# Kernel optimization log

Measured on AMD Instinct MI355X. Metric: run time of the kernel, lower is better.

## Reference

```python
import jax, jax.numpy as jnp
import numpy as np

DIM = 1024
LN_EPS = 1e-5


def setup_inputs() -> dict:
    key = jax.random.key(0)
    ks = jax.random.split(key, 6)
    B, S, D = 8, 2048, DIM
    x = jax.random.normal(ks[0], (B, S, D), dtype=jnp.float32)
    mask = jnp.ones((B, S, 1), dtype=jnp.float32)
    # LayerNorm params
    ln_g = jnp.ones((D,), dtype=jnp.float32)
    ln_b = jnp.zeros((D,), dtype=jnp.float32)
    # FeedForward: Linear(D, D) -> GELU -> Linear(D, D); hidden_dim == dim per source
    lim = 1.0 / np.sqrt(D)
    w1 = jax.random.uniform(ks[1], (D, D), jnp.float32, -lim, lim)
    b1 = jax.random.uniform(ks[2], (D,), jnp.float32, -lim, lim)
    w2 = jax.random.uniform(ks[3], (D, D), jnp.float32, -lim, lim)
    b2 = jax.random.uniform(ks[4], (D,), jnp.float32, -lim, lim)
    return {"x": x, "mask": mask, "ln_g": ln_g, "ln_b": ln_b,
            "w1": w1, "b1": b1, "w2": w2, "b2": b2}


def _layernorm(t, g, b):
    mu = jnp.mean(t, axis=-1, keepdims=True)
    var = jnp.mean(jnp.square(t - mu), axis=-1, keepdims=True)
    return (t - mu) * jax.lax.rsqrt(var + LN_EPS) * g + b


def reference(x, mask, ln_g, ln_b, w1, b1, w2, b2):
    # torch.fft(t, signal_ndim=1): FFT over hidden axis (complex input, imag=0)
    ft = jnp.fft.fft(x.astype(jnp.float32), axis=-1)
    # torch.fft(., signal_ndim=2): 2D FFT over (seq, hidden)
    ft = jnp.fft.fft2(ft, axes=(-2, -1))
    ft = ft.real  # [..., 0] slice of the fake-complex tensor
    t = _layernorm(x + ft, ln_g, ln_b)
    # FeedForward: Linear -> GELU(exact) -> Linear (dropout is identity at eval)
    h = jax.nn.gelu(t @ w1 + b1, approximate=False)
    out = h @ w2 + b2
    return out * mask
```

## Files before the change

kernel.cpp:

```cpp
#include <hip/hip_runtime.h>
#include <math.h>

#define DIMD 1024
#define SEQ  2048
#define BATCH 8
#define ROWS (BATCH * SEQ)

#define MF 1152
#define KF 1088

typedef __attribute__((ext_vector_type(8))) short bf16x8;
typedef __attribute__((ext_vector_type(4))) float f32x4;
typedef __attribute__((ext_vector_type(8))) unsigned short ushort8;

__device__ __forceinline__ unsigned short f2bf(float f) {
    unsigned u = __float_as_uint(f);
    unsigned r = (u + 0x7FFFu + ((u >> 16) & 1u)) >> 16;
    return (unsigned short)r;
}
__device__ __forceinline__ void gl_lds16(const void* g, void* l) {
    __builtin_amdgcn_global_load_lds(
        (const __attribute__((address_space(1))) unsigned int*)g,
        (__attribute__((address_space(3))) unsigned int*)l, 16, 0, 0);
}


__global__ __launch_bounds__(256) void build_acos(unsigned short* __restrict__ Acos) {
    int s = blockIdx.x;
    for (int t = threadIdx.x; t < KF; t += 256) {
        float c = 0.0f;
        if (t <= 1024) {
            int prod = (s * t) & (SEQ - 1);
            c = cospif((float)prod * (1.0f / 1024.0f));
        }
        Acos[(size_t)s * KF + t] = f2bf(c);
    }
}

__global__ __launch_bounds__(256) void build_xe(const float* __restrict__ x,
                                                unsigned short* __restrict__ Xe) {
    int lane = threadIdx.x & 63;
    int oct  = threadIdx.x >> 6;
    int n = blockIdx.x * 64 + lane;
    int b = n >> 10, d = n & 1023;
    int rd = (DIMD - d) & (DIMD - 1);
    int t0 = blockIdx.y * 32 + oct * 8;
    const float* xb = x + (size_t)b * SEQ * DIMD + rd;
    ushort8 tmp;
    #pragma unroll
    for (int j = 0; j < 8; ++j) {
        int t = t0 + j;
        float v;
        if (t == 0)          v = xb[0];
        else if (t < 1024)   v = xb[(size_t)t * DIMD] + xb[(size_t)(2048 - t) * DIMD];
        else if (t == 1024)  v = xb[(size_t)1024 * DIMD];
        else                 v = 0.0f;
        tmp[j] = f2bf(v);
    }
    *(ushort8*)&Xe[(size_t)n * KF + t0] = tmp;
}

__global__ __launch_bounds__(256) void pack_wt(const float* __restrict__ W,
                                               unsigned short* __restrict__ Wt) {
    int lane = threadIdx.x & 63;
    int oct = threadIdx.x >> 6;
    int n = blockIdx.x * 64 + lane;
    int k0 = blockIdx.y * 32 + oct * 8;
    ushort8 tmp;
    #pragma unroll
    for (int j = 0; j < 8; ++j) tmp[j] = f2bf(W[(size_t)(k0 + j) * DIMD + n]);
    *(ushort8*)&Wt[(size_t)n * DIMD + k0] = tmp;
}

template <int MODE>
__global__ __launch_bounds__(256) void gemm_bt(const unsigned short* __restrict__ A,
                                               const unsigned short* __restrict__ B,
                                               int K, int lda, int ldb, int ldc,
                                               const float* __restrict__ bias,
                                               const float* __restrict__ mask,
                                               void* __restrict__ outp) {
    __shared__ unsigned short As[128 * 64];
    __shared__ unsigned short Bs[128 * 64];

    const int tid = threadIdx.x;
    const int lane = tid & 63;
    const int wv = tid >> 6;
    const int wm = wv & 1;
    const int wn = wv >> 1;
    const int fr = lane & 15;
    const int quad = lane >> 4;

    const int m0 = blockIdx.y * 128;
    const int n0 = blockIdx.x * 128;

    const int st_row = (lane >> 3);
    const int st_col = (lane & 7) * 8;

    f32x4 acc[4][4] = {};

    for (int k0 = 0; k0 < K; k0 += 64) {
        __syncthreads();
        #pragma unroll
        for (int i = 0; i < 4; ++i) {
            int chunk = wv * 4 + i;
            int ar = m0 + chunk * 8 + st_row;
            int br = n0 + chunk * 8 + st_row;
            gl_lds16(&A[(size_t)ar * lda + k0 + st_col], &As[chunk * 512]);
            gl_lds16(&B[(size_t)br * ldb + k0 + st_col], &Bs[chunk * 512]);
        }
        __syncthreads();

        #pragma unroll
        for (int ks = 0; ks < 2; ++ks) {
            bf16x8 af[4], bfv[4];
            #pragma unroll
            for (int i = 0; i < 4; ++i)
                af[i] = *(const bf16x8*)&As[(wm * 64 + i * 16 + fr) * 64 + ks * 32 + quad * 8];
            #pragma unroll
            for (int j = 0; j < 4; ++j)
                bfv[j] = *(const bf16x8*)&Bs[(wn * 64 + j * 16 + fr) * 64 + ks * 32 + quad * 8];
            #pragma unroll
            for (int i = 0; i < 4; ++i)
                #pragma unroll
                for (int j = 0; j < 4; ++j)
                    acc[i][j] = __builtin_amdgcn_mfma_f32_16x16x32_bf16(af[i], bfv[j], acc[i][j], 0, 0, 0);
        }
    }

    #pragma unroll
    for (int i = 0; i < 4; ++i) {
        int rowb = m0 + wm * 64 + i * 16 + quad * 4;
        #pragma unroll
        for (int j = 0; j < 4; ++j) {
            int col = n0 + wn * 64 + j * 16 + fr;
            #pragma unroll
            for (int r = 0; r < 4; ++r) {
                float v = acc[i][j][r];
                int row = rowb + r;
                if (MODE == 0) {
                    ((float*)outp)[(size_t)row * ldc + col] = v;
                } else if (MODE == 1) {
                    v += bias[col];
                    v = 0.5f * v * (1.0f + erff(v * 0.70710678118654752f));
                    ((unsigned short*)outp)[(size_t)row * ldc + col] = f2bf(v);
                } else {
                    v += bias[col];
                    v *= mask[row];
                    ((float*)outp)[(size_t)row * ldc + col] = v;
                }
            }
        }
    }
}

__global__ __launch_bounds__(256) void ln_mirror(const float* __restrict__ x,
                                                 const float* __restrict__ F,
                                                 const float* __restrict__ g,
                                                 const float* __restrict__ beta,
                                                 unsigned short* __restrict__ t) {
    const int row = blockIdx.x;
    const int b = row >> 11, s = row & 2047;
    const int sp = (s <= 1024) ? s : (2048 - s);

    float4 xv = ((const float4*)(x + (size_t)row * DIMD))[threadIdx.x];
    float4 fv = ((const float4*)(F + (size_t)sp * 8192 + (size_t)b * 1024))[threadIdx.x];
    float4 v;
    v.x = xv.x + 1024.0f * fv.x;
    v.y = xv.y + 1024.0f * fv.y;
    v.z = xv.z + 1024.0f * fv.z;
    v.w = xv.w + 1024.0f * fv.w;

    __shared__ float red[4];
    const int wave = threadIdx.x >> 6;
    const int lane = threadIdx.x & 63;

    float sm = v.x + v.y + v.z + v.w;
    #pragma unroll
    for (int off = 32; off > 0; off >>= 1) sm += __shfl_down(sm, off, 64);
    if (lane == 0) red[wave] = sm;
    __syncthreads();
    const float mean = (red[0] + red[1] + red[2] + red[3]) * (1.0f / DIMD);

    float dx0 = v.x - mean, dx1 = v.y - mean, dx2 = v.z - mean, dx3 = v.w - mean;
    float q = dx0 * dx0 + dx1 * dx1 + dx2 * dx2 + dx3 * dx3;
    __syncthreads();
    #pragma unroll
    for (int off = 32; off > 0; off >>= 1) q += __shfl_down(q, off, 64);
    if (lane == 0) red[wave] = q;
    __syncthreads();
    const float var = (red[0] + red[1] + red[2] + red[3]) * (1.0f / DIMD);
    const float rstd = rsqrtf(var + 1e-5f);

    float4 g4 = ((const float4*)g)[threadIdx.x];
    float4 b4 = ((const float4*)beta)[threadIdx.x];
    ushort4 o;
    o.x = f2bf(dx0 * rstd * g4.x + b4.x);
    o.y = f2bf(dx1 * rstd * g4.y + b4.y);
    o.z = f2bf(dx2 * rstd * g4.z + b4.z);
    o.w = f2bf(dx3 * rstd * g4.w + b4.w);
    ((ushort4*)(t + (size_t)row * DIMD))[threadIdx.x] = o;
}

#define BM 64
#define BN 64
#define BK 16

__global__ __launch_bounds__(256) void fft_cos_kernel(const float* __restrict__ x,
                                                      float* __restrict__ y) {
    __shared__ float tab[SEQ];
    __shared__ float As[BM][BK + 1];
    __shared__ float Bs[BK][BN + 1];
    const int tid = threadIdx.x;
    const int b = blockIdx.z;
    const int s0 = blockIdx.y * BM;
    const int n0 = blockIdx.x * BN;
    for (int i = tid; i < SEQ; i += 256) tab[i] = cospif((float)i * (1.0f / 1024.0f));
    const int tx = tid & 15;
    const int ty = tid >> 4;
    float acc[4][4] = {};
    const float* Xb = x + (size_t)b * SEQ * DIMD;
    for (int k0 = 0; k0 < SEQ; k0 += BK) {
        __syncthreads();
        for (int f = tid; f < BM * BK; f += 256) {
            int i = f / BK, k = f % BK;
            int prod = (s0 + i) * (k0 + k);
            As[i][k] = tab[prod & (SEQ - 1)];
        }
        for (int f = tid; f < BK * BN; f += 256) {
            int k = f / BN, j = f % BN;
            int d = n0 + j;
            int rd = (DIMD - d) & (DIMD - 1);
            Bs[k][j] = Xb[(size_t)(k0 + k) * DIMD + rd];
        }
        __syncthreads();
        #pragma unroll
        for (int k = 0; k < BK; ++k) {
            float a[4], bv[4];
            #pragma unroll
            for (int i = 0; i < 4; ++i) a[i] = As[ty * 4 + i][k];
            #pragma unroll
            for (int j = 0; j < 4; ++j) bv[j] = Bs[k][tx * 4 + j];
            #pragma unroll
            for (int i = 0; i < 4; ++i)
                #pragma unroll
                for (int j = 0; j < 4; ++j) acc[i][j] += a[i] * bv[j];
        }
    }
    #pragma unroll
    for (int i = 0; i < 4; ++i) {
        int s = s0 + ty * 4 + i;
        #pragma unroll
        for (int j = 0; j < 4; ++j) {
            int d = n0 + tx * 4 + j;
            y[((size_t)b * SEQ + s) * DIMD + d] = Xb[(size_t)s * DIMD + d] + 1024.0f * acc[i][j];
        }
    }
}

__global__ __launch_bounds__(256) void ln_kernel(float* __restrict__ y,
                                                 const float* __restrict__ g,
                                                 const float* __restrict__ beta) {
    const int row = blockIdx.x;
    float4* p = (float4*)(y + (size_t)row * DIMD);
    float4 v = p[threadIdx.x];
    __shared__ float red[4];
    const int wave = threadIdx.x >> 6;
    const int lane = threadIdx.x & 63;
    float s = v.x + v.y + v.z + v.w;
    #pragma unroll
    for (int off = 32; off > 0; off >>= 1) s += __shfl_down(s, off, 64);
    if (lane == 0) red[wave] = s;
    __syncthreads();
    const float mean = (red[0] + red[1] + red[2] + red[3]) * (1.0f / DIMD);
    float dx0 = v.x - mean, dx1 = v.y - mean, dx2 = v.z - mean, dx3 = v.w - mean;
    float q = dx0 * dx0 + dx1 * dx1 + dx2 * dx2 + dx3 * dx3;
    __syncthreads();
    #pragma unroll
    for (int off = 32; off > 0; off >>= 1) q += __shfl_down(q, off, 64);
    if (lane == 0) red[wave] = q;
    __syncthreads();
    const float var = (red[0] + red[1] + red[2] + red[3]) * (1.0f / DIMD);
    const float rstd = rsqrtf(var + 1e-5f);
    float4 g4 = ((const float4*)g)[threadIdx.x];
    float4 b4 = ((const float4*)beta)[threadIdx.x];
    float4 o;
    o.x = dx0 * rstd * g4.x + b4.x;
    o.y = dx1 * rstd * g4.y + b4.y;
    o.z = dx2 * rstd * g4.z + b4.z;
    o.w = dx3 * rstd * g4.w + b4.w;
    p[threadIdx.x] = o;
}

template <int MODE>
__global__ __launch_bounds__(256) void ff_gemm(const float* __restrict__ A,
                                               const float* __restrict__ W,
                                               const float* __restrict__ bias,
                                               const float* __restrict__ mask,
                                               float* __restrict__ out) {
    __shared__ float As[BM][BK + 1];
    __shared__ float Bs[BK][BN + 1];
    const int tid = threadIdx.x;
    const int tx = tid & 15;
    const int ty = tid >> 4;
    const int m0 = blockIdx.y * BM;
    const int n0 = blockIdx.x * BN;
    float acc[4][4] = {};
    for (int k0 = 0; k0 < DIMD; k0 += BK) {
        __syncthreads();
        for (int f = tid; f < BM * BK; f += 256) {
            int i = f / BK, k = f % BK;
            As[i][k] = A[(size_t)(m0 + i) * DIMD + k0 + k];
        }
        for (int f = tid; f < BK * BN; f += 256) {
            int k = f / BN, j = f % BN;
            Bs[k][j] = W[(size_t)(k0 + k) * DIMD + n0 + j];
        }
        __syncthreads();
        #pragma unroll
        for (int k = 0; k < BK; ++k) {
            float a[4], bv[4];
            #pragma unroll
            for (int i = 0; i < 4; ++i) a[i] = As[ty * 4 + i][k];
            #pragma unroll
            for (int j = 0; j < 4; ++j) bv[j] = Bs[k][tx * 4 + j];
            #pragma unroll
            for (int i = 0; i < 4; ++i)
                #pragma unroll
                for (int j = 0; j < 4; ++j) acc[i][j] += a[i] * bv[j];
        }
    }
    #pragma unroll
    for (int i = 0; i < 4; ++i) {
        int m = m0 + ty * 4 + i;
        float mk = (MODE == 1) ? mask[m] : 1.0f;
        #pragma unroll
        for (int j = 0; j < 4; ++j) {
            int n = n0 + tx * 4 + j;
            float v = acc[i][j] + bias[n];
            if (MODE == 0) v = 0.5f * v * (1.0f + erff(v * 0.70710678118654752f));
            else v *= mk;
            out[(size_t)m * DIMD + n] = v;
        }
    }
}

extern "C" void kernel_launch(void* const* d_in, const int* in_sizes, int n_in,
                              void* d_out, int out_size, void* d_ws, size_t ws_size,
                              hipStream_t stream) {
    const float* x    = (const float*)d_in[0];
    const float* mask = (const float*)d_in[1];
    const float* ln_g = (const float*)d_in[2];
    const float* ln_b = (const float*)d_in[3];
    const float* w1   = (const float*)d_in[4];
    const float* b1   = (const float*)d_in[5];
    const float* w2   = (const float*)d_in[6];
    const float* b2   = (const float*)d_in[7];
    float* out = (float*)d_out;

    const size_t MB = 1024 * 1024;
    dim3 blk(256);

    if (ws_size >= 70 * MB) {
        char* w = (char*)d_ws;
        unsigned short* Acos = (unsigned short*)w;
        unsigned short* Xe   = (unsigned short*)(w + 4 * MB);
        unsigned short* t    = (unsigned short*)(w + 32 * MB);
        unsigned short* W1t  = (unsigned short*)(w + 64 * MB);
        unsigned short* W2t  = (unsigned short*)(w + 66 * MB);
        unsigned short* h    = (unsigned short*)w;
        float* F = (float*)d_out;

        build_acos<<<dim3(MF), blk, 0, stream>>>(Acos);
        build_xe<<<dim3(8192 / 64, KF / 32), blk, 0, stream>>>(x, Xe);
        pack_wt<<<dim3(1024 / 64, 1024 / 32), blk, 0, stream>>>(w1, W1t);
        pack_wt<<<dim3(1024 / 64, 1024 / 32), blk, 0, stream>>>(w2, W2t);

        gemm_bt<0><<<dim3(8192 / 128, MF / 128), blk, 0, stream>>>(
            Acos, Xe, KF, KF, KF, 8192, nullptr, nullptr, F);
        ln_mirror<<<dim3(ROWS), blk, 0, stream>>>(x, F, ln_g, ln_b, t);
        gemm_bt<1><<<dim3(1024 / 128, ROWS / 128), blk, 0, stream>>>(
            t, W1t, 1024, 1024, 1024, 1024, b1, nullptr, h);
        gemm_bt<2><<<dim3(1024 / 128, ROWS / 128), blk, 0, stream>>>(
            h, W2t, 1024, 1024, 1024, 1024, b2, mask, out);
    } else {
        float* y = (float*)d_ws;
        const size_t bufBytes = (size_t)ROWS * DIMD * sizeof(float);
        fft_cos_kernel<<<dim3(DIMD / BN, SEQ / BM, BATCH), blk, 0, stream>>>(x, y);
        ln_kernel<<<dim3(ROWS), blk, 0, stream>>>(y, ln_g, ln_b);
        ff_gemm<0><<<dim3(DIMD / BN, ROWS / BM), blk, 0, stream>>>(y, w1, b1, nullptr, out);
        ff_gemm<1><<<dim3(DIMD / BN, ROWS / BM), blk, 0, stream>>>(out, w2, b2, mask, y);
        hipMemcpyAsync(d_out, y, bufBytes, hipMemcpyDeviceToDevice, stream);
    }
}
```

Measured before the change: 344.6 us.

## Fuse residual add and mirror expansion into DFT GEMM epilogue with bf16 output

The DFT GEMM epilogue now adds the input residual scaled spectrum directly and writes both the row and its mirrored row as bf16. This removes the fp32 intermediate F buffer and its re-read in LayerNorm, which now only reads a bf16 row. The FFN GEMMs also get a grouped block index remap to improve L2 reuse of A tiles. The trade-offs are that the pre-LN activations are rounded to bf16, and that the epilogue does scattered loads of x with narrow 16-bit stores.

Measured after the change: 380.4 us. 1.1x slower.

```diff
diff --git a/kernel.cpp b/kernel.cpp
--- a/kernel.cpp
+++ b/kernel.cpp
@@ -17,6 +17,9 @@
     unsigned u = __float_as_uint(f);
     unsigned r = (u + 0x7FFFu + ((u >> 16) & 1u)) >> 16;
     return (unsigned short)r;
+}
+__device__ __forceinline__ float bf2f(unsigned short h) {
+    return __uint_as_float(((unsigned)h) << 16);
 }
 __device__ __forceinline__ void gl_lds16(const void* g, void* l) {
     __builtin_amdgcn_global_load_lds(
@@ -76,6 +79,7 @@
 __global__ __launch_bounds__(256) void gemm_bt(const unsigned short* __restrict__ A,
                                                const unsigned short* __restrict__ B,
                                                int K, int lda, int ldb, int ldc,
+                                               const float* __restrict__ xres,
                                                const float* __restrict__ bias,
                                                const float* __restrict__ mask,
                                                void* __restrict__ outp) {
@@ -90,8 +94,16 @@
     const int fr = lane & 15;
     const int quad = lane >> 4;
 
-    const int m0 = blockIdx.y * 128;
-    const int n0 = blockIdx.x * 128;
+    int bx = blockIdx.x, by = blockIdx.y;
+    if (MODE != 0) {
+        int lin = bx + 8 * by;
+        int c = lin & 7;
+        int g = lin >> 3;
+        bx = g & 7;
+        by = (g >> 3) * 8 + c;
+    }
+    const int m0 = by * 128;
+    const int n0 = bx * 128;
 
     const int st_row = (lane >> 3);
     const int st_col = (lane & 7) * 8;
@@ -138,7 +150,17 @@
                 float v = acc[i][j][r];
                 int row = rowb + r;
                 if (MODE == 0) {
-                    ((float*)outp)[(size_t)row * ldc + col] = v;
+                    int s = row;
+                    if (s <= 1024) {
+                        int b = col >> 10, d = col & 1023;
+                        unsigned short* y = (unsigned short*)outp;
+                        size_t i1 = ((size_t)b * SEQ + s) * DIMD + d;
+                        y[i1] = f2bf(xres[i1] + 1024.0f * v);
+                        if (s >= 1 && s <= 1023) {
+                            size_t i2 = ((size_t)b * SEQ + (2048 - s)) * DIMD + d;
+                            y[i2] = f2bf(xres[i2] + 1024.0f * v);
+                        }
+                    }
                 } else if (MODE == 1) {
                     v += bias[col];
                     v = 0.5f * v * (1.0f + erff(v * 0.70710678118654752f));
@@ -153,35 +175,26 @@
     }
 }
 
-__global__ __launch_bounds__(256) void ln_mirror(const float* __restrict__ x,
-                                                 const float* __restrict__ F,
-                                                 const float* __restrict__ g,
-                                                 const float* __restrict__ beta,
-                                                 unsigned short* __restrict__ t) {
+__global__ __launch_bounds__(256) void ln_bf(const unsigned short* __restrict__ y,
+                                             const float* __restrict__ g,
+                                             const float* __restrict__ beta,
+                                             unsigned short* __restrict__ t) {
     const int row = blockIdx.x;
-    const int b = row >> 11, s = row & 2047;
-    const int sp = (s <= 1024) ? s : (2048 - s);
-
-    float4 xv = ((const float4*)(x + (size_t)row * DIMD))[threadIdx.x];
-    float4 fv = ((const float4*)(F + (size_t)sp * 8192 + (size_t)b * 1024))[threadIdx.x];
-    float4 v;
-    v.x = xv.x + 1024.0f * fv.x;
-    v.y = xv.y + 1024.0f * fv.y;
-    v.z = xv.z + 1024.0f * fv.z;
-    v.w = xv.w + 1024.0f * fv.w;
+    ushort4 raw = ((const ushort4*)(y + (size_t)row * DIMD))[threadIdx.x];
+    float v0 = bf2f(raw.x), v1 = bf2f(raw.y), v2 = bf2f(raw.z), v3 = bf2f(raw.w);
 
     __shared__ float red[4];
     const int wave = threadIdx.x >> 6;
     const int lane = threadIdx.x & 63;
 
-    float sm = v.x + v.y + v.z + v.w;
+    float sm = v0 + v1 + v2 + v3;
     #pragma unroll
     for (int off = 32; off > 0; off >>= 1) sm += __shfl_down(sm, off, 64);
     if (lane == 0) red[wave] = sm;
     __syncthreads();
     const float mean = (red[0] + red[1] + red[2] + red[3]) * (1.0f / DIMD);
 
-    float dx0 = v.x - mean, dx1 = v.y - mean, dx2 = v.z - mean, dx3 = v.w - mean;
+    float dx0 = v0 - mean, dx1 = v1 - mean, dx2 = v2 - mean, dx3 = v3 - mean;
     float q = dx0 * dx0 + dx1 * dx1 + dx2 * dx2 + dx3 * dx3;
     __syncthreads();
     #pragma unroll
@@ -364,11 +377,11 @@
         char* w = (char*)d_ws;
         unsigned short* Acos = (unsigned short*)w;
         unsigned short* Xe   = (unsigned short*)(w + 4 * MB);
-        unsigned short* t    = (unsigned short*)(w + 32 * MB);
+        unsigned short* y    = (unsigned short*)(w + 32 * MB);
+        unsigned short* t    = (unsigned short*)w;
+        unsigned short* h    = (unsigned short*)(w + 32 * MB);
         unsigned short* W1t  = (unsigned short*)(w + 64 * MB);
         unsigned short* W2t  = (unsigned short*)(w + 66 * MB);
-        unsigned short* h    = (unsigned short*)w;
-        float* F = (float*)d_out;
 
         build_acos<<<dim3(MF), blk, 0, stream>>>(Acos);
         build_xe<<<dim3(8192 / 64, KF / 32), blk, 0, stream>>>(x, Xe);
@@ -376,19 +389,19 @@
         pack_wt<<<dim3(1024 / 64, 1024 / 32), blk, 0, stream>>>(w2, W2t);
 
         gemm_bt<0><<<dim3(8192 / 128, MF / 128), blk, 0, stream>>>(
-            Acos, Xe, KF, KF, KF, 8192, nullptr, nullptr, F);
-        ln_mirror<<<dim3(ROWS), blk, 0, stream>>>(x, F, ln_g, ln_b, t);
+            Acos, Xe, KF, KF, KF, 0, x, nullptr, nullptr, y);
+        ln_bf<<<dim3(ROWS), blk, 0, stream>>>(y, ln_g, ln_b, t);
         gemm_bt<1><<<dim3(1024 / 128, ROWS / 128), blk, 0, stream>>>(
-            t, W1t, 1024, 1024, 1024, 1024, b1, nullptr, h);
+            t, W1t, 1024, 1024, 1024, 1024, nullptr, b1, nullptr, h);
         gemm_bt<2><<<dim3(1024 / 128, ROWS / 128), blk, 0, stream>>>(
-            h, W2t, 1024, 1024, 1024, 1024, b2, mask, out);
+            h, W2t, 1024, 1024, 1024, 1024, nullptr, b2, mask, out);
     } else {
-        float* y = (float*)d_ws;
+        float* yf = (float*)d_ws;
         const size_t bufBytes = (size_t)ROWS * DIMD * sizeof(float);
-        fft_cos_kernel<<<dim3(DIMD / BN, SEQ / BM, BATCH), blk, 0, stream>>>(x, y);
-        ln_kernel<<<dim3(ROWS), blk, 0, stream>>>(y, ln_g, ln_b);
-        ff_gemm<0><<<dim3(DIMD / BN, ROWS / BM), blk, 0, stream>>>(y, w1, b1, nullptr, out);
-        ff_gemm<1><<<dim3(DIMD / BN, ROWS / BM), blk, 0, stream>>>(out, w2, b2, mask, y);
-        hipMemcpyAsync(d_out, y, bufBytes, hipMemcpyDeviceToDevice, stream);
-    }
-}
+        fft_cos_kernel<<<dim3(DIMD / BN, SEQ / BM, BATCH), blk, 0, stream>>>(x, yf);
+        ln_kernel<<<dim3(ROWS), blk, 0, stream>>>(yf, ln_g, ln_b);
+        ff_gemm<0><<<dim3(DIMD / BN, ROWS / BM), blk, 0, stream>>>(yf, w1, b1, nullptr, out);
+        ff_gemm<1><<<dim3(DIMD / BN, ROWS / BM), blk, 0, stream>>>(out, w2, b2, mask, yf);
+        hipMemcpyAsync(d_out, yf, bufBytes, hipMemcpyDeviceToDevice, stream);
+    }
+}
```
